# Optimization experiments

Measured on AMD Instinct MI355X. Metric: run time of the kernel, lower is better.

Reference implementation:

```python
import jax, jax.numpy as jnp
import numpy as np

B, L, DIM, H, D = 2, 2048, 1024, 16, 64


def setup_inputs() -> dict:
    key = jax.random.key(0)
    ks = jax.random.split(key, 20)
    s = 1.0 / np.sqrt(DIM)
    inp = {
        "query": jax.random.normal(ks[0], (B, L, DIM), jnp.float32),
        "keys": jax.random.normal(ks[1], (B, L, DIM), jnp.float32),
        "values": jax.random.normal(ks[2], (B, L, DIM), jnp.float32),
        "focus_vector": jax.random.normal(ks[3], (B, DIM), jnp.float32),
        "temporal_weights": jax.random.normal(ks[4], (B, L), jnp.float32),
        "importance_weights": jax.random.normal(ks[5], (B, L), jnp.float32),
        # linear params, stored [in, out] for x @ W + b
        "Wq": jax.random.normal(ks[6], (DIM, H * D), jnp.float32) * s,
        "bq": jnp.zeros((H * D,), jnp.float32),
        "Wk": jax.random.normal(ks[7], (DIM, H * D), jnp.float32) * s,
        "bk": jnp.zeros((H * D,), jnp.float32),
        "Wv": jax.random.normal(ks[8], (DIM, H * D), jnp.float32) * s,
        "bv": jnp.zeros((H * D,), jnp.float32),
        "Wp": jax.random.normal(ks[9], (H * D, DIM), jnp.float32) * s,
        "bp": jnp.zeros((DIM,), jnp.float32),
        "Wt": jax.random.normal(ks[10], (DIM, 1), jnp.float32) * s,
        "bt": jnp.zeros((1,), jnp.float32),
        "Wi": jax.random.normal(ks[11], (DIM, 1), jnp.float32) * s,
        "bi": jnp.zeros((1,), jnp.float32),
    }
    return inp


def reference(query, keys, values, focus_vector, temporal_weights, importance_weights,
              Wq, bq, Wk, bk, Wv, bv, Wp, bp, Wt, bt, Wi, bi):
    b, l, _ = query.shape
    # QKV projections -> [B, H, L, D]
    q = (query @ Wq + bq).reshape(b, l, H, D).transpose(0, 2, 1, 3)
    k = (keys @ Wk + bk).reshape(b, -1, H, D).transpose(0, 2, 1, 3)
    v = (values @ Wv + bv).reshape(b, -1, H, D).transpose(0, 2, 1, 3)
    scores = jnp.einsum("bhqd,bhkd->bhqk", q, k) / np.sqrt(D).astype(np.float32)
    # gate-modulated weights over keys [B, Lk]
    temporal_scores = (keys @ Wt + bt)[..., 0]
    tw = jax.nn.softmax(temporal_scores * temporal_weights, axis=-1)
    importance_scores = (keys @ Wi + bi)[..., 0]
    iw = jax.nn.softmax(importance_scores * importance_weights, axis=-1)
    rw = jax.nn.softmax(jnp.einsum("bkd,bd->bk", keys, focus_vector), axis=-1)
    combined = (tw + iw + rw) / 3.0
    scores = scores * combined[:, None, None, :]
    weights = jax.nn.softmax(scores, axis=-1)  # dropout is identity in eval
    out = jnp.einsum("bhqk,bhkd->bhqd", weights, v)
    out = out.transpose(0, 2, 1, 3).reshape(b, l, H * D)
    out = out @ Wp + bp
    return out, weights
```

## Files before the change

### kernel.cpp

```cpp
#include <hip/hip_runtime.h>
#include <hip/hip_bf16.h>
#include <cstdint>

#define DEV static __device__ __forceinline__

typedef __attribute__((ext_vector_type(8))) short short8_;
typedef __attribute__((ext_vector_type(4))) float float4_;
typedef __attribute__((ext_vector_type(4))) float f4v;
typedef __attribute__((ext_vector_type(4))) unsigned short u16x4;
typedef __attribute__((ext_vector_type(2))) uint32_t u32x2;
typedef unsigned short u16;

constexpr int Bb   = 2;
constexpr int Ls   = 2048;
constexpr int DIMc = 1024;
constexpr int Hh   = 16;
constexpr int Dd   = 64;
constexpr int BL   = Bb * Ls;
constexpr int HD   = Hh * Dd;

DEV u16 f2bf(float f) {
  union { float f; uint32_t u; } v; v.f = f;
  return (u16)((v.u + 0x7fffu + ((v.u >> 16) & 1u)) >> 16);
}

DEV float4_ mfma16(short8_ a, short8_ b, float4_ c) {
  return __builtin_amdgcn_mfma_f32_16x16x32_bf16(a, b, c, 0, 0, 0);
}

DEV void gload_lds16(const void* g, void* l) {
  __builtin_amdgcn_global_load_lds(
      (const __attribute__((address_space(1))) void*)g,
      (__attribute__((address_space(3))) void*)l, 16, 0, 0);
}

__global__ void k_prep(const float* __restrict__ query, const float* __restrict__ keys,
                       const float* __restrict__ values, u16* __restrict__ qx,
                       u16* __restrict__ kx, u16* __restrict__ vx,
                       const float* __restrict__ Wq, const float* __restrict__ Wk,
                       const float* __restrict__ Wv, const float* __restrict__ Wp,
                       u16* __restrict__ WqT, u16* __restrict__ WkT,
                       u16* __restrict__ WvT, u16* __restrict__ WpT,
                       const float* __restrict__ Wt, const float* __restrict__ bt,
                       const float* __restrict__ Wi, const float* __restrict__ bi,
                       const float* __restrict__ focus,
                       float* __restrict__ ts, float* __restrict__ is_,
                       float* __restrict__ rs) {
  __shared__ float t[64][65];
  const int bid = blockIdx.x, tid = threadIdx.x;
  if (bid < 12288) {
    int z = bid >> 12;
    const float* s = (z == 0) ? query : (z == 1) ? keys : values;
    u16* d = (z == 0) ? qx : (z == 1) ? kx : vx;
    int i = (bid & 4095) * 256 + tid;
    f4v v = ((const f4v*)s)[i];
    u16x4 o = { f2bf(v[0]), f2bf(v[1]), f2bf(v[2]), f2bf(v[3]) };
    ((u16x4*)d)[i] = o;
  } else if (bid < 13312) {
    int r2 = bid - 12288;
    int z = r2 >> 8, rem = r2 & 255;
    const float* W = (z == 0) ? Wq : (z == 1) ? Wk : (z == 2) ? Wv : Wp;
    u16* WT = (z == 0) ? WqT : (z == 1) ? WkT : (z == 2) ? WvT : WpT;
    int n0 = (rem >> 4) * 64, k0 = (rem & 15) * 64;
    int tx = tid & 63, tg = tid >> 6;
#pragma unroll
    for (int i = 0; i < 16; ++i) {
      int r = tg * 16 + i;
      t[r][tx] = W[(size_t)(k0 + r) * HD + n0 + tx];
    }
    __syncthreads();
#pragma unroll
    for (int i = 0; i < 16; ++i) {
      int r = tg * 16 + i;
      WT[(size_t)(n0 + r) * DIMc + k0 + tx] = f2bf(t[tx][r]);
    }
  } else {
    int wv = tid >> 6, ln = tid & 63;
    int row = (bid - 13312) * 4 + wv;
    int b = row >> 11;
    const float* kr = keys + (size_t)row * DIMc;
    const float* fr = focus + (size_t)b * DIMc;
    float st = 0.f, si = 0.f, sr = 0.f;
    for (int j = ln; j < DIMc; j += 64) {
      float kv = kr[j];
      st += kv * Wt[j]; si += kv * Wi[j]; sr += kv * fr[j];
    }
#pragma unroll
    for (int m = 1; m < 64; m <<= 1) {
      st += __shfl_xor(st, m); si += __shfl_xor(si, m); sr += __shfl_xor(sr, m);
    }
    if (ln == 0) { ts[row] = st + bt[0]; is_[row] = si + bi[0]; rs[row] = sr; }
  }
}

__global__ void k_combined(const float* __restrict__ ts, const float* __restrict__ is_,
                           const float* __restrict__ rs, const float* __restrict__ tw,
                           const float* __restrict__ iw, float* __restrict__ comb) {
  int b = blockIdx.x, t = threadIdx.x;
  __shared__ float red[3][4];
  float lt[8], li[8], lr[8];
  float m3[3] = {-1e30f, -1e30f, -1e30f};
#pragma unroll
  for (int i = 0; i < 8; ++i) {
    int gi = b * Ls + i * 256 + t;
    lt[i] = ts[gi] * tw[gi];
    li[i] = is_[gi] * iw[gi];
    lr[i] = rs[gi];
    m3[0] = fmaxf(m3[0], lt[i]); m3[1] = fmaxf(m3[1], li[i]); m3[2] = fmaxf(m3[2], lr[i]);
  }
#pragma unroll
  for (int q = 0; q < 3; ++q) {
    float v = m3[q];
#pragma unroll
    for (int m = 32; m; m >>= 1) v = fmaxf(v, __shfl_xor(v, m));
    if ((t & 63) == 0) red[q][t >> 6] = v;
  }
  __syncthreads();
#pragma unroll
  for (int q = 0; q < 3; ++q)
    m3[q] = fmaxf(fmaxf(red[q][0], red[q][1]), fmaxf(red[q][2], red[q][3]));
  __syncthreads();
  float s3[3] = {0.f, 0.f, 0.f};
#pragma unroll
  for (int i = 0; i < 8; ++i) {
    lt[i] = __expf(lt[i] - m3[0]); s3[0] += lt[i];
    li[i] = __expf(li[i] - m3[1]); s3[1] += li[i];
    lr[i] = __expf(lr[i] - m3[2]); s3[2] += lr[i];
  }
#pragma unroll
  for (int q = 0; q < 3; ++q) {
    float v = s3[q];
#pragma unroll
    for (int m = 32; m; m >>= 1) v += __shfl_xor(v, m);
    if ((t & 63) == 0) red[q][t >> 6] = v;
  }
  __syncthreads();
#pragma unroll
  for (int q = 0; q < 3; ++q) s3[q] = red[q][0] + red[q][1] + red[q][2] + red[q][3];
  float rt = 1.f / s3[0], ri = 1.f / s3[1], rr = 1.f / s3[2];
  const float scl = (1.f / 3.f) * 0.125f;
#pragma unroll
  for (int i = 0; i < 8; ++i) {
    int gi = b * Ls + i * 256 + t;
    comb[gi] = (lt[i] * rt + li[i] * ri + lr[i] * rr) * scl;
  }
}

__launch_bounds__(256, 3)
__global__ void k_gemm_qkv(const u16* __restrict__ qx, const u16* __restrict__ kx,
                           const u16* __restrict__ vx, const u16* __restrict__ WqT,
                           const u16* __restrict__ WkT, const u16* __restrict__ WvT,
                           const float* __restrict__ bq, const float* __restrict__ bk,
                           const float* __restrict__ bv, u16* __restrict__ q_bh,
                           u16* __restrict__ k_bh, u16* __restrict__ vT) {
  __shared__ __align__(16) u16 As[128 * 32];
  __shared__ __align__(16) u16 Bs[128 * 32];
  const int z = blockIdx.z;
  const u16* A  = (z == 0) ? qx : (z == 1) ? kx : vx;
  const u16* BT = (z == 0) ? WqT : (z == 1) ? WkT : WvT;
  const float* bias = (z == 0) ? bq : (z == 1) ? bk : bv;
  const int tid = threadIdx.x, wv = tid >> 6, ln = tid & 63;
  const int g = ln >> 4, c = ln & 15;
  const int m0 = blockIdx.x * 128, n0 = blockIdx.y * 128;
  const int wm = wv >> 1, wn = wv & 1;
  const float4_ z4 = {0.f, 0.f, 0.f, 0.f};
  float4_ acc[4][4];
#pragma unroll
  for (int i = 0; i < 4; ++i)
#pragma unroll
    for (int j = 0; j < 4; ++j) acc[i][j] = z4;
  const int lrow = ln >> 2, lcol = (ln & 3) * 8;
  for (int k0 = 0; k0 < 1024; k0 += 32) {
#pragma unroll
    for (int s = 0; s < 2; ++s) {
      int r0 = wv * 32 + s * 16;
      gload_lds16(A  + (size_t)(m0 + r0 + lrow) * 1024 + k0 + lcol, &As[r0 * 32]);
      gload_lds16(BT + (size_t)(n0 + r0 + lrow) * 1024 + k0 + lcol, &Bs[r0 * 32]);
    }
    __syncthreads();
    short8_ af[4], bfr[4];
#pragma unroll
    for (int mt = 0; mt < 4; ++mt)
      af[mt] = *(const short8_*)&As[(wm * 64 + mt * 16 + c) * 32 + g * 8];
#pragma unroll
    for (int nt = 0; nt < 4; ++nt)
      bfr[nt] = *(const short8_*)&Bs[(wn * 64 + nt * 16 + c) * 32 + g * 8];
#pragma unroll
    for (int mt = 0; mt < 4; ++mt)
#pragma unroll
      for (int nt = 0; nt < 4; ++nt)
        acc[mt][nt] = mfma16(af[mt], bfr[nt], acc[mt][nt]);
    __syncthreads();
  }
  if (z < 2) {
    u16* Q = (z == 0) ? q_bh : k_bh;
#pragma unroll
    for (int mt = 0; mt < 4; ++mt)
#pragma unroll
      for (int nt = 0; nt < 4; ++nt) {
        int n = n0 + wn * 64 + nt * 16 + c;
        float bv_ = bias[n];
        int h = n >> 6, d = n & 63;
#pragma unroll
        for (int r = 0; r < 4; ++r) {
          int m = m0 + wm * 64 + mt * 16 + g * 4 + r;
          int b = m >> 11, l = m & 2047;
          Q[((size_t)((b * Hh + h) * Ls + l)) * Dd + d] = f2bf(acc[mt][nt][r] + bv_);
        }
      }
  } else {
#pragma unroll
    for (int mt = 0; mt < 4; ++mt)
#pragma unroll
      for (int nt = 0; nt < 4; ++nt) {
        int n = n0 + wn * 64 + nt * 16 + c;
        float bv_ = bias[n];
        int h = n >> 6, d = n & 63;
        int mrow = m0 + wm * 64 + mt * 16 + g * 4;
        int b = mrow >> 11, l = mrow & 2047;
        u16x4 o = { f2bf(acc[mt][nt][0] + bv_), f2bf(acc[mt][nt][1] + bv_),
                    f2bf(acc[mt][nt][2] + bv_), f2bf(acc[mt][nt][3] + bv_) };
        *(u16x4*)&vT[((size_t)((b * Hh + h) * Dd + d)) * Ls + l] = o;
      }
  }
}

__launch_bounds__(256, 4)
__global__ void k_attn4(const u16* __restrict__ q_bh, const u16* __restrict__ k_bh,
                        const u16* __restrict__ vT, const float* __restrict__ comb_g,
                        float* __restrict__ wout, u16* __restrict__ ctx) {
  __shared__ __align__(16) u16 Kt[2][64][64];
  __shared__ __align__(16) u16 Vt[2][64][64];
  __shared__ __align__(16) uint32_t Ew[4][16][32];

  const int bid = blockIdx.x;
  const int logical = (bid & 7) * 128 + (bid >> 3);
  const int bh = logical >> 5, qb = logical & 31;
  const int b = bh >> 4, h = bh & 15;
  const int l0 = qb * 64;
  const int w = threadIdx.x >> 6, ln = threadIdx.x & 63;
  const int g = ln >> 4, c = ln & 15;
  const int srow = ln >> 3, x8 = ln & 7;
  const float4_ z4 = {0.f, 0.f, 0.f, 0.f};

  const u16* kbh = k_bh + (size_t)bh * Ls * Dd;
  const u16* vbh = vT + (size_t)bh * Dd * Ls;
  const float* kcomb = comb_g + (size_t)b * Ls;

  const u16* qp = q_bh + ((size_t)bh * Ls + l0 + w * 16) * Dd;
  short8_ aq0 = *(const short8_*)&qp[c * Dd + g * 8];
  short8_ aq1 = *(const short8_*)&qp[c * Dd + 32 + g * 8];

  auto stageK = [&](int buf, int kb) {
#pragma unroll
    for (int i = 0; i < 2; ++i) {
      int rr = w * 16 + i * 8 + srow;
      int sc = (x8 ^ (rr & 7)) * 8;
      gload_lds16(kbh + (size_t)(kb + rr) * Dd + sc, &Kt[buf][w * 16 + i * 8][0]);
    }
  };
  auto stageV = [&](int buf, int kb) {
#pragma unroll
    for (int i = 0; i < 2; ++i) {
      int rr = w * 16 + i * 8 + srow;
      int sc = (x8 ^ (rr & 7)) * 8;
      gload_lds16(vbh + (size_t)rr * Ls + kb + sc, &Vt[buf][w * 16 + i * 8][0]);
    }
  };

  float4_ accO[4];
#pragma unroll
  for (int dt = 0; dt < 4; ++dt) accO[dt] = z4;
  float rs_loc = 0.f;

  stageK(0, 0); stageV(0, 0);
  __syncthreads();

  int buf = 0;
  for (int t = 0; t < 32; ++t) {
    if (t < 31) { stageK(buf ^ 1, (t + 1) * 64); stageV(buf ^ 1, (t + 1) * 64); }
    const int kb = t * 64;
#pragma unroll
    for (int s = 0; s < 4; ++s) {
      int rowK = s * 16 + c;
      short8_ bk0 = *(const short8_*)&Kt[buf][rowK][((g    ) ^ (c & 7)) * 8];
      short8_ bk1 = *(const short8_*)&Kt[buf][rowK][((4 + g) ^ (c & 7)) * 8];
      float4_ st = mfma16(bk0, aq0, z4);
      st = mfma16(bk1, aq1, st);
      float4_ cc4 = *(const float4_*)&kcomb[kb + s * 16 + g * 4];
      float e0 = __expf(st[0] * cc4[0]);
      float e1 = __expf(st[1] * cc4[1]);
      float e2 = __expf(st[2] * cc4[2]);
      float e3 = __expf(st[3] * cc4[3]);
      rs_loc += (e0 + e1) + (e2 + e3);
      uint32_t lo = ((uint32_t)f2bf(e1) << 16) | f2bf(e0);
      uint32_t hi = ((uint32_t)f2bf(e3) << 16) | f2bf(e2);
      int chunk = (s * 2 + (g >> 1)) ^ (c & 7);
      u32x2 pk = { lo, hi };
      *(u32x2*)&Ew[w][c][chunk * 4 + (g & 1) * 2] = pk;
    }
#pragma unroll
    for (int hf = 0; hf < 2; ++hf) {
      short8_ ea = *(const short8_*)&Ew[w][c][((hf * 4 + g) ^ (c & 7)) * 4];
#pragma unroll
      for (int dt = 0; dt < 4; ++dt) {
        short8_ bv = *(const short8_*)&Vt[buf][dt * 16 + c][((hf * 4 + g) ^ (c & 7)) * 8];
        accO[dt] = mfma16(ea, bv, accO[dt]);
      }
    }
    __syncthreads();
    buf ^= 1;
  }

  rs_loc += __shfl_xor(rs_loc, 16);
  rs_loc += __shfl_xor(rs_loc, 32);
  float inv = 1.0f / rs_loc;
  float invrow[4];
#pragma unroll
  for (int r = 0; r < 4; ++r) invrow[r] = __shfl(inv, g * 4 + r);

  u16* out_lds = &Vt[0][0][0] + w * 1152;
#pragma unroll
  for (int dt = 0; dt < 4; ++dt)
#pragma unroll
    for (int r = 0; r < 4; ++r)
      out_lds[(g * 4 + r) * 72 + dt * 16 + c] = f2bf(accO[dt][r] * invrow[r]);
  {
    int rr2 = ln >> 2, sg = ln & 3;
    short8_ d0 = *(const short8_*)&out_lds[rr2 * 72 + sg * 16];
    short8_ d1 = *(const short8_*)&out_lds[rr2 * 72 + sg * 16 + 8];
    u16* cp = ctx + ((size_t)(b * Ls + l0 + w * 16 + rr2)) * HD + h * Dd + sg * 16;
    *(short8_*)cp = d0;
    *(short8_*)(cp + 8) = d1;
  }

  stageK(0, 0);
  __syncthreads();
  buf = 0;
  float* wb = wout + ((size_t)bh * Ls + l0 + w * 16) * Ls;
  for (int t = 0; t < 32; ++t) {
    if (t < 31) stageK(buf ^ 1, (t + 1) * 64);
    const int kb = t * 64;
#pragma unroll
    for (int s = 0; s < 4; ++s) {
      int rowK = s * 16 + c;
      short8_ bk0 = *(const short8_*)&Kt[buf][rowK][((g    ) ^ (c & 7)) * 8];
      short8_ bk1 = *(const short8_*)&Kt[buf][rowK][((4 + g) ^ (c & 7)) * 8];
      float4_ st = mfma16(bk0, aq0, z4);
      st = mfma16(bk1, aq1, st);
      float4_ cc4 = *(const float4_*)&kcomb[kb + s * 16 + g * 4];
      float4_ o;
#pragma unroll
      for (int r = 0; r < 4; ++r) o[r] = __expf(st[r] * cc4[r]) * inv;
      *(float4_*)&wb[(size_t)c * Ls + kb + s * 16 + g * 4] = o;
    }
    __syncthreads();
    buf ^= 1;
  }
}

__launch_bounds__(256, 4)
__global__ void k_gemmO(const u16* __restrict__ A, const u16* __restrict__ BT,
                        const float* __restrict__ bias, float* __restrict__ O) {
  __shared__ __align__(16) u16 As[64 * 32];
  __shared__ __align__(16) u16 Bs[128 * 32];
  const int tid = threadIdx.x, wv = tid >> 6, ln = tid & 63;
  const int g = ln >> 4, c = ln & 15;
  const int m0 = blockIdx.x * 64, n0 = blockIdx.y * 128;
  const int wm = wv >> 1, wn = wv & 1;
  const float4_ z4 = {0.f, 0.f, 0.f, 0.f};
  float4_ acc[2][4];
#pragma unroll
  for (int i = 0; i < 2; ++i)
#pragma unroll
    for (int j = 0; j < 4; ++j) acc[i][j] = z4;
  const int lrow = ln >> 2, lcol = (ln & 3) * 8;
  for (int k0 = 0; k0 < 1024; k0 += 32) {
    gload_lds16(A + (size_t)(m0 + wv * 16 + lrow) * 1024 + k0 + lcol, &As[(wv * 16) * 32]);
#pragma unroll
    for (int s = 0; s < 2; ++s) {
      int r0 = wv * 32 + s * 16;
      gload_lds16(BT + (size_t)(n0 + r0 + lrow) * 1024 + k0 + lcol, &Bs[r0 * 32]);
    }
    __syncthreads();
    short8_ af[2], bfr[4];
#pragma unroll
    for (int mt = 0; mt < 2; ++mt)
      af[mt] = *(const short8_*)&As[(wm * 32 + mt * 16 + c) * 32 + g * 8];
#pragma unroll
    for (int nt = 0; nt < 4; ++nt)
      bfr[nt] = *(const short8_*)&Bs[(wn * 64 + nt * 16 + c) * 32 + g * 8];
#pragma unroll
    for (int mt = 0; mt < 2; ++mt)
#pragma unroll
      for (int nt = 0; nt < 4; ++nt)
        acc[mt][nt] = mfma16(af[mt], bfr[nt], acc[mt][nt]);
    __syncthreads();
  }
#pragma unroll
  for (int mt = 0; mt < 2; ++mt)
#pragma unroll
    for (int nt = 0; nt < 4; ++nt) {
      int n = n0 + wn * 64 + nt * 16 + c;
      float bv_ = bias[n];
#pragma unroll
      for (int r = 0; r < 4; ++r) {
        int m = m0 + wm * 32 + mt * 16 + g * 4 + r;
        O[(size_t)m * HD + n] = acc[mt][nt][r] + bv_;
      }
    }
}

extern "C" void kernel_launch(void* const* d_in, const int* in_sizes, int n_in,
                              void* d_out, int out_size, void* d_ws, size_t ws_size,
                              hipStream_t stream) {
  (void)in_sizes; (void)n_in; (void)out_size; (void)ws_size;
  const float* query = (const float*)d_in[0];
  const float* keys  = (const float*)d_in[1];
  const float* values= (const float*)d_in[2];
  const float* focus = (const float*)d_in[3];
  const float* twg   = (const float*)d_in[4];
  const float* iwg   = (const float*)d_in[5];
  const float* Wq = (const float*)d_in[6];  const float* bq = (const float*)d_in[7];
  const float* Wk = (const float*)d_in[8];  const float* bk = (const float*)d_in[9];
  const float* Wv = (const float*)d_in[10]; const float* bv = (const float*)d_in[11];
  const float* Wp = (const float*)d_in[12]; const float* bp = (const float*)d_in[13];
  const float* Wt = (const float*)d_in[14]; const float* bt = (const float*)d_in[15];
  const float* Wi = (const float*)d_in[16]; const float* bi = (const float*)d_in[17];

  char* ws = (char*)d_ws;
  size_t off = 0;
  auto alloc = [&](size_t bytes) -> char* {
    char* p = ws + off; off += (bytes + 255) & ~(size_t)255; return p;
  };
  const size_t NTOK = (size_t)BL * DIMc;
  u16* qx   = (u16*)alloc(NTOK * 2);
  u16* kx   = (u16*)alloc(NTOK * 2);
  u16* vx   = (u16*)alloc(NTOK * 2);
  u16* WqT  = (u16*)alloc((size_t)DIMc * HD * 2);
  u16* WkT  = (u16*)alloc((size_t)DIMc * HD * 2);
  u16* WvT  = (u16*)alloc((size_t)DIMc * HD * 2);
  u16* WpT  = (u16*)alloc((size_t)DIMc * HD * 2);
  u16* q_bh = (u16*)alloc(NTOK * 2);
  u16* k_bh = (u16*)alloc(NTOK * 2);
  u16* vTb  = (u16*)alloc(NTOK * 2);
  u16* ctx  = (u16*)alloc(NTOK * 2);
  float* ts   = (float*)alloc((size_t)BL * 4);
  float* is_  = (float*)alloc((size_t)BL * 4);
  float* rs   = (float*)alloc((size_t)BL * 4);
  float* comb = (float*)alloc((size_t)BL * 4);

  float* out_f = (float*)d_out;
  float* w_out = out_f + (size_t)BL * HD;

  k_prep<<<14336, 256, 0, stream>>>(query, keys, values, qx, kx, vx,
                                    Wq, Wk, Wv, Wp, WqT, WkT, WvT, WpT,
                                    Wt, bt, Wi, bi, focus, ts, is_, rs);
  k_combined<<<2, 256, 0, stream>>>(ts, is_, rs, twg, iwg, comb);
  dim3 gq(32, 8, 3);
  k_gemm_qkv<<<gq, 256, 0, stream>>>(qx, kx, vx, WqT, WkT, WvT, bq, bk, bv,
                                     q_bh, k_bh, vTb);
  k_attn4<<<1024, 256, 0, stream>>>(q_bh, k_bh, vTb, comb, w_out, ctx);
  dim3 go(64, 8);
  k_gemmO<<<go, 256, 0, stream>>>(ctx, WpT, bp, out_f);
}
```

Measured before the change: 293.6 us.

## Process two 16-row query tiles per wave in attention to reuse K/V tiles

Each wave in the attention kernel now handles 32 query rows instead of 16, so every block covers 128 queries and the grid drops from 1024 to 512 blocks. Each K and V fragment loaded from LDS feeds twice as many MFMAs, and K/V global staging per query is halved. The cost is more registers (launch bounds lowered to 3 blocks per CU), a larger LDS exp buffer, and fewer blocks to spread over the CUs. The attention-weights output write, probably the dominant memory cost, is unchanged.

```diff
diff --git a/kernel.cpp b/kernel.cpp
--- a/kernel.cpp
+++ b/kernel.cpp
@@ -225,19 +225,19 @@
   }
 }
 
-__launch_bounds__(256, 4)
-__global__ void k_attn4(const u16* __restrict__ q_bh, const u16* __restrict__ k_bh,
+__launch_bounds__(256, 3)
+__global__ void k_attn5(const u16* __restrict__ q_bh, const u16* __restrict__ k_bh,
                         const u16* __restrict__ vT, const float* __restrict__ comb_g,
                         float* __restrict__ wout, u16* __restrict__ ctx) {
   __shared__ __align__(16) u16 Kt[2][64][64];
   __shared__ __align__(16) u16 Vt[2][64][64];
-  __shared__ __align__(16) uint32_t Ew[4][16][32];
+  __shared__ __align__(16) uint32_t Ew[4][2][16][32];
 
   const int bid = blockIdx.x;
-  const int logical = (bid & 7) * 128 + (bid >> 3);
-  const int bh = logical >> 5, qb = logical & 31;
+  const int logical = (bid & 7) * 64 + (bid >> 3);
+  const int bh = logical >> 4, qb = logical & 15;
   const int b = bh >> 4, h = bh & 15;
-  const int l0 = qb * 64;
+  const int l0 = qb * 128;
   const int w = threadIdx.x >> 6, ln = threadIdx.x & 63;
   const int g = ln >> 4, c = ln & 15;
   const int srow = ln >> 3, x8 = ln & 7;
@@ -247,9 +247,11 @@
   const u16* vbh = vT + (size_t)bh * Dd * Ls;
   const float* kcomb = comb_g + (size_t)b * Ls;
 
-  const u16* qp = q_bh + ((size_t)bh * Ls + l0 + w * 16) * Dd;
-  short8_ aq0 = *(const short8_*)&qp[c * Dd + g * 8];
-  short8_ aq1 = *(const short8_*)&qp[c * Dd + 32 + g * 8];
+  const u16* qp = q_bh + ((size_t)bh * Ls + l0 + w * 32) * Dd;
+  short8_ aq00 = *(const short8_*)&qp[c * Dd + g * 8];
+  short8_ aq01 = *(const short8_*)&qp[c * Dd + 32 + g * 8];
+  short8_ aq10 = *(const short8_*)&qp[(16 + c) * Dd + g * 8];
+  short8_ aq11 = *(const short8_*)&qp[(16 + c) * Dd + 32 + g * 8];
 
   auto stageK = [&](int buf, int kb) {
 #pragma unroll
@@ -268,10 +270,12 @@
     }
   };
 
-  float4_ accO[4];
-#pragma unroll
-  for (int dt = 0; dt < 4; ++dt) accO[dt] = z4;
-  float rs_loc = 0.f;
+  float4_ accO[2][4];
+#pragma unroll
+  for (int blk = 0; blk < 2; ++blk)
+#pragma unroll
+    for (int dt = 0; dt < 4; ++dt) accO[blk][dt] = z4;
+  float rs0 = 0.f, rs1 = 0.f;
 
   stageK(0, 0); stageV(0, 0);
   __syncthreads();
@@ -285,51 +289,68 @@
       int rowK = s * 16 + c;
       short8_ bk0 = *(const short8_*)&Kt[buf][rowK][((g    ) ^ (c & 7)) * 8];
       short8_ bk1 = *(const short8_*)&Kt[buf][rowK][((4 + g) ^ (c & 7)) * 8];
-      float4_ st = mfma16(bk0, aq0, z4);
-      st = mfma16(bk1, aq1, st);
       float4_ cc4 = *(const float4_*)&kcomb[kb + s * 16 + g * 4];
-      float e0 = __expf(st[0] * cc4[0]);
-      float e1 = __expf(st[1] * cc4[1]);
-      float e2 = __expf(st[2] * cc4[2]);
-      float e3 = __expf(st[3] * cc4[3]);
-      rs_loc += (e0 + e1) + (e2 + e3);
-      uint32_t lo = ((uint32_t)f2bf(e1) << 16) | f2bf(e0);
-      uint32_t hi = ((uint32_t)f2bf(e3) << 16) | f2bf(e2);
       int chunk = (s * 2 + (g >> 1)) ^ (c & 7);
-      u32x2 pk = { lo, hi };
-      *(u32x2*)&Ew[w][c][chunk * 4 + (g & 1) * 2] = pk;
+      int ewo = chunk * 4 + (g & 1) * 2;
+      float4_ st0 = mfma16(bk0, aq00, z4);
+      st0 = mfma16(bk1, aq01, st0);
+      float4_ st1 = mfma16(bk0, aq10, z4);
+      st1 = mfma16(bk1, aq11, st1);
+      {
+        float e0 = __expf(st0[0] * cc4[0]), e1 = __expf(st0[1] * cc4[1]);
+        float e2 = __expf(st0[2] * cc4[2]), e3 = __expf(st0[3] * cc4[3]);
+        rs0 += (e0 + e1) + (e2 + e3);
+        u32x2 pk = { ((uint32_t)f2bf(e1) << 16) | f2bf(e0),
+                     ((uint32_t)f2bf(e3) << 16) | f2bf(e2) };
+        *(u32x2*)&Ew[w][0][c][ewo] = pk;
+      }
+      {
+        float e0 = __expf(st1[0] * cc4[0]), e1 = __expf(st1[1] * cc4[1]);
+        float e2 = __expf(st1[2] * cc4[2]), e3 = __expf(st1[3] * cc4[3]);
+        rs1 += (e0 + e1) + (e2 + e3);
+        u32x2 pk = { ((uint32_t)f2bf(e1) << 16) | f2bf(e0),
+                     ((uint32_t)f2bf(e3) << 16) | f2bf(e2) };
+        *(u32x2*)&Ew[w][1][c][ewo] = pk;
+      }
     }
 #pragma unroll
     for (int hf = 0; hf < 2; ++hf) {
-      short8_ ea = *(const short8_*)&Ew[w][c][((hf * 4 + g) ^ (c & 7)) * 4];
+      int eo = ((hf * 4 + g) ^ (c & 7)) * 4;
+      short8_ ea0 = *(const short8_*)&Ew[w][0][c][eo];
+      short8_ ea1 = *(const short8_*)&Ew[w][1][c][eo];
 #pragma unroll
       for (int dt = 0; dt < 4; ++dt) {
         short8_ bv = *(const short8_*)&Vt[buf][dt * 16 + c][((hf * 4 + g) ^ (c & 7)) * 8];
-        accO[dt] = mfma16(ea, bv, accO[dt]);
+        accO[0][dt] = mfma16(ea0, bv, accO[0][dt]);
+        accO[1][dt] = mfma16(ea1, bv, accO[1][dt]);
       }
     }
     __syncthreads();
     buf ^= 1;
   }
 
-  rs_loc += __shfl_xor(rs_loc, 16);
-  rs_loc += __shfl_xor(rs_loc, 32);
-  float inv = 1.0f / rs_loc;
-  float invrow[4];
-#pragma unroll
-  for (int r = 0; r < 4; ++r) invrow[r] = __shfl(inv, g * 4 + r);
+  rs0 += __shfl_xor(rs0, 16); rs0 += __shfl_xor(rs0, 32);
+  rs1 += __shfl_xor(rs1, 16); rs1 += __shfl_xor(rs1, 32);
+  float inv0 = 1.0f / rs0, inv1 = 1.0f / rs1;
+  float invrow[2][4];
+#pragma unroll
+  for (int r = 0; r < 4; ++r) {
+    invrow[0][r] = __shfl(inv0, g * 4 + r);
+    invrow[1][r] = __shfl(inv1, g * 4 + r);
+  }
 
   u16* out_lds = &Vt[0][0][0] + w * 1152;
 #pragma unroll
-  for (int dt = 0; dt < 4; ++dt)
-#pragma unroll
-    for (int r = 0; r < 4; ++r)
-      out_lds[(g * 4 + r) * 72 + dt * 16 + c] = f2bf(accO[dt][r] * invrow[r]);
-  {
+  for (int blk = 0; blk < 2; ++blk) {
+#pragma unroll
+    for (int dt = 0; dt < 4; ++dt)
+#pragma unroll
+      for (int r = 0; r < 4; ++r)
+        out_lds[(g * 4 + r) * 72 + dt * 16 + c] = f2bf(accO[blk][dt][r] * invrow[blk][r]);
     int rr2 = ln >> 2, sg = ln & 3;
     short8_ d0 = *(const short8_*)&out_lds[rr2 * 72 + sg * 16];
     short8_ d1 = *(const short8_*)&out_lds[rr2 * 72 + sg * 16 + 8];
-    u16* cp = ctx + ((size_t)(b * Ls + l0 + w * 16 + rr2)) * HD + h * Dd + sg * 16;
+    u16* cp = ctx + ((size_t)(b * Ls + l0 + w * 32 + blk * 16 + rr2)) * HD + h * Dd + sg * 16;
     *(short8_*)cp = d0;
     *(short8_*)(cp + 8) = d1;
   }
@@ -337,7 +358,7 @@
   stageK(0, 0);
   __syncthreads();
   buf = 0;
-  float* wb = wout + ((size_t)bh * Ls + l0 + w * 16) * Ls;
+  float* wb = wout + ((size_t)bh * Ls + l0 + w * 32) * Ls;
   for (int t = 0; t < 32; ++t) {
     if (t < 31) stageK(buf ^ 1, (t + 1) * 64);
     const int kb = t * 64;
@@ -346,13 +367,20 @@
       int rowK = s * 16 + c;
       short8_ bk0 = *(const short8_*)&Kt[buf][rowK][((g    ) ^ (c & 7)) * 8];
       short8_ bk1 = *(const short8_*)&Kt[buf][rowK][((4 + g) ^ (c & 7)) * 8];
-      float4_ st = mfma16(bk0, aq0, z4);
-      st = mfma16(bk1, aq1, st);
       float4_ cc4 = *(const float4_*)&kcomb[kb + s * 16 + g * 4];
-      float4_ o;
-#pragma unroll
-      for (int r = 0; r < 4; ++r) o[r] = __expf(st[r] * cc4[r]) * inv;
-      *(float4_*)&wb[(size_t)c * Ls + kb + s * 16 + g * 4] = o;
+      float4_ st0 = mfma16(bk0, aq00, z4);
+      st0 = mfma16(bk1, aq01, st0);
+      float4_ st1 = mfma16(bk0, aq10, z4);
+      st1 = mfma16(bk1, aq11, st1);
+      float4_ o0, o1;
+#pragma unroll
+      for (int r = 0; r < 4; ++r) {
+        o0[r] = __expf(st0[r] * cc4[r]) * inv0;
+        o1[r] = __expf(st1[r] * cc4[r]) * inv1;
+      }
+      int col = kb + s * 16 + g * 4;
+      *(float4_*)&wb[(size_t)c * Ls + col] = o0;
+      *(float4_*)&wb[(size_t)(16 + c) * Ls + col] = o1;
     }
     __syncthreads();
     buf ^= 1;
@@ -460,7 +488,7 @@
   dim3 gq(32, 8, 3);
   k_gemm_qkv<<<gq, 256, 0, stream>>>(qx, kx, vx, WqT, WkT, WvT, bq, bk, bv,
                                      q_bh, k_bh, vTb);
-  k_attn4<<<1024, 256, 0, stream>>>(q_bh, k_bh, vTb, comb, w_out, ctx);
+  k_attn5<<<512, 256, 0, stream>>>(q_bh, k_bh, vTb, comb, w_out, ctx);
   dim3 go(64, 8);
   k_gemmO<<<go, 256, 0, stream>>>(ctx, WpT, bp, out_f);
 }
```

Result: slower. 304.9 us (+3.8%).
